# Kernel optimization log

Hardware: AMD Instinct MI355X
Metric: run time of the kernel (lower is better)

## Reference

```python
import jax, jax.numpy as jnp
import numpy as np

N = 100_000      # nodes
E = 1_600_000    # directed edges (avg degree 16)
F_IN = 128       # num_node_features
H = 8            # heads in conv1
C = 32           # hidden_channels
G = 64           # graphs in batch
NC = 10          # num_classes


def setup_inputs() -> dict:
    key = jax.random.key(0)
    ks = jax.random.split(key, 12)
    gl = lambda k, shape, fan: (jax.random.normal(k, shape, jnp.float32) / np.sqrt(fan)).astype(jnp.float32)
    return {
        "x": jax.random.normal(ks[0], (N, F_IN), jnp.float32),
        "edge_index": jax.random.randint(ks[1], (2, E), 0, N, dtype=jnp.int32),
        "batch": jnp.sort(jax.random.randint(ks[2], (N,), 0, G, dtype=jnp.int32)),
        "W1": gl(ks[3], (F_IN, H * C), F_IN),
        "att_src1": gl(ks[4], (H, C), C),
        "att_dst1": gl(ks[5], (H, C), C),
        "b1": jnp.zeros((H * C,), jnp.float32),
        "W2": gl(ks[6], (H * C, C), H * C),
        "att_src2": gl(ks[7], (1, C), C),
        "att_dst2": gl(ks[8], (1, C), C),
        "b2": jnp.zeros((C,), jnp.float32),
        "Wlin": gl(ks[9], (C, NC), C),
        "blin": jnp.zeros((NC,), jnp.float32),
    }


def gat_conv(x, src, dst, W, att_src, att_dst, bias, heads, ch, concat):
    """PyG GATConv (eval mode): gather, LeakyReLU(0.2) scores, segment softmax over dst, scatter-sum."""
    n = x.shape[0]
    h = (x @ W).reshape(n, heads, ch)                     # [N,H,C]
    a_s = jnp.sum(h * att_src, axis=-1)                   # [N,H]
    a_d = jnp.sum(h * att_dst, axis=-1)                   # [N,H]
    e = jax.nn.leaky_relu(a_s[src] + a_d[dst], 0.2)       # [E,H]
    m = jax.ops.segment_max(e, dst, num_segments=n)       # [N,H], stable softmax
    p = jnp.exp(e - m[dst])
    z = jax.ops.segment_sum(p, dst, num_segments=n)
    coef = p / (z[dst] + 1e-16)                           # [E,H]
    out = jax.ops.segment_sum(coef[:, :, None] * h[src], dst, num_segments=n)  # [N,H,C]
    out = out.reshape(n, heads * ch) if concat else out.mean(axis=1)
    return out + bias


def reference(x, edge_index, batch, W1, att_src1, att_dst1, b1,
              W2, att_src2, att_dst2, b2, Wlin, blin):
    n = x.shape[0]
    loops = jnp.arange(n, dtype=edge_index.dtype)         # GATConv add_self_loops=True
    src = jnp.concatenate([edge_index[0], loops])
    dst = jnp.concatenate([edge_index[1], loops])

    h = gat_conv(x, src, dst, W1, att_src1, att_dst1, b1, H, C, concat=True)
    h = jax.nn.elu(h)                                     # dropout is identity in eval
    h = gat_conv(h, src, dst, W2, att_src2, att_dst2, b2, 1, C, concat=False)

    # global_mean_pool over graph ids
    sums = jax.ops.segment_sum(h, batch, num_segments=G)  # [G,C]
    cnts = jax.ops.segment_sum(jnp.ones((n,), h.dtype), batch, num_segments=G)
    pooled = sums / jnp.maximum(cnts, 1.0)[:, None]

    return pooled @ Wlin + blin                           # [G,NC]
```

## Files before the change

kernel.cpp:

```cpp
#include <hip/hip_runtime.h>
#include <cstdint>

#define NN 100000
#define EE 1600000
#define GG 64
#define FIN 128
#define HC 256
#define NC 10

typedef short v8s __attribute__((ext_vector_type(8)));
typedef float v4f __attribute__((ext_vector_type(4)));
typedef unsigned short u8s __attribute__((ext_vector_type(8)));

static __device__ __forceinline__ float lrelu(float x) { return x > 0.f ? x : 0.2f * x; }
static __device__ __forceinline__ float bf2f(unsigned short b) {
  return __uint_as_float(((unsigned int)b) << 16);
}
static __device__ __forceinline__ unsigned short f2bf(float f) {
  unsigned int u = __float_as_uint(f);
  unsigned int r = (u + 0x7FFFu + ((u >> 16) & 1u)) >> 16;
  return (unsigned short)r;
}
static __device__ __forceinline__ void unpack2(unsigned int u, float& f0, float& f1) {
  f0 = __uint_as_float(u << 16);
  f1 = __uint_as_float(u & 0xFFFF0000u);
}

__global__ __launch_bounds__(256) void k_prepall(const float* __restrict__ x,
                                                 unsigned short* __restrict__ xb,
                                                 const int* __restrict__ ei,
                                                 int* __restrict__ counts,
                                                 const float* __restrict__ W1,
                                                 unsigned short* __restrict__ W1tg,
                                                 const float* __restrict__ W2,
                                                 unsigned short* __restrict__ W2thi,
                                                 unsigned short* __restrict__ W2tlo) {
  const int b = blockIdx.x;
  const int t = threadIdx.x;
  if (b < 12500) {
    const int idx = b * 256 + t;
    const int i4 = idx * 4;
    float4 v = *(const float4*)(x + i4);
    ushort4 u;
    u.x = f2bf(v.x); u.y = f2bf(v.y); u.z = f2bf(v.z); u.w = f2bf(v.w);
    *(ushort4*)(xb + i4) = u;
    if (idx < EE) atomicAdd(&counts[ei[EE + idx]], 1);
  } else if (b < 12756) {
    const int n = b - 12500;
    if (t < 128) W1tg[n * 128 + t] = f2bf(W1[t * HC + n]);
  } else {
    const int oc = b - 12756;
    float wv = W2[t * 32 + oc];
    unsigned short hi = f2bf(wv);
    W2thi[oc * 256 + t] = hi;
    W2tlo[oc * 256 + t] = f2bf(wv - bf2f(hi));
  }
}

__global__ __launch_bounds__(256) void k_gemm1(const unsigned short* __restrict__ xb,
                                               const unsigned short* __restrict__ W1tg,
                                               const float* __restrict__ att_src1,
                                               const float* __restrict__ att_dst1,
                                               unsigned short* __restrict__ h1b,
                                               float* __restrict__ as1,
                                               float* __restrict__ ad1) {
  const int t = threadIdx.x;
  const int m0 = blockIdx.x * 64;
  const int n0 = blockIdx.y * 128;
  const int hb = blockIdx.y * 4;
  const int lane = t & 63;
  const int wm = t >> 6;
  const int ml = lane & 15;
  const int quad = lane >> 4;
  int row = m0 + wm * 16 + ml; if (row >= NN) row = NN - 1;
  v4f acc[8];
#pragma unroll
  for (int tt = 0; tt < 8; ++tt) acc[tt] = (v4f){0.f, 0.f, 0.f, 0.f};
#pragma unroll
  for (int kk = 0; kk < 4; ++kk) {
    const int k0 = kk * 32 + quad * 8;
    v8s a = *(const v8s*)(xb + (size_t)row * FIN + k0);
#pragma unroll
    for (int tt = 0; tt < 8; ++tt) {
      v8s b = *(const v8s*)(W1tg + (size_t)(n0 + tt * 16 + ml) * FIN + k0);
      acc[tt] = __builtin_amdgcn_mfma_f32_16x16x32_bf16(a, b, acc[tt], 0, 0, 0);
    }
  }
#pragma unroll
  for (int tt = 0; tt < 8; ++tt) {
#pragma unroll
    for (int r = 0; r < 4; ++r) {
      int rg = m0 + wm * 16 + quad * 4 + r;
      if (rg < NN) h1b[(size_t)rg * HC + n0 + tt * 16 + ml] = f2bf(acc[tt][r]);
    }
  }
  float ps[4][4], pd[4][4];
#pragma unroll
  for (int i = 0; i < 4; ++i)
#pragma unroll
    for (int r = 0; r < 4; ++r) { ps[i][r] = 0.f; pd[i][r] = 0.f; }
#pragma unroll
  for (int i = 0; i < 4; ++i) {
#pragma unroll
    for (int half = 0; half < 2; ++half) {
      const int tt = 2 * i + half;
      const float a_s = att_src1[(hb + i) * 32 + half * 16 + ml];
      const float a_d = att_dst1[(hb + i) * 32 + half * 16 + ml];
#pragma unroll
      for (int r = 0; r < 4; ++r) {
        ps[i][r] += acc[tt][r] * a_s;
        pd[i][r] += acc[tt][r] * a_d;
      }
    }
  }
#pragma unroll
  for (int i = 0; i < 4; ++i) {
#pragma unroll
    for (int r = 0; r < 4; ++r) {
      float s = ps[i][r], d = pd[i][r];
      s += __shfl_xor(s, 1, 64); s += __shfl_xor(s, 2, 64);
      s += __shfl_xor(s, 4, 64); s += __shfl_xor(s, 8, 64);
      d += __shfl_xor(d, 1, 64); d += __shfl_xor(d, 2, 64);
      d += __shfl_xor(d, 4, 64); d += __shfl_xor(d, 8, 64);
      ps[i][r] = s; pd[i][r] = d;
    }
  }
  if (ml == 0) {
#pragma unroll
    for (int r = 0; r < 4; ++r) {
      int rg = m0 + wm * 16 + quad * 4 + r;
      if (rg < NN) {
#pragma unroll
        for (int i = 0; i < 4; ++i) {
          as1[rg * 8 + hb + i] = ps[i][r];
          ad1[rg * 8 + hb + i] = pd[i][r];
        }
      }
    }
  }
}

__global__ void k_scan1(const int* __restrict__ counts, int* __restrict__ offs,
                        int* __restrict__ bsums) {
  __shared__ int s[256];
  const int t = threadIdx.x;
  const int i = blockIdx.x * 256 + t;
  int v = (i < NN) ? counts[i] : 0;
  s[t] = v;
  __syncthreads();
  for (int off = 1; off < 256; off <<= 1) {
    int tv = (t >= off) ? s[t - off] : 0;
    __syncthreads();
    s[t] += tv;
    __syncthreads();
  }
  if (i < NN) offs[i] = s[t] - v;
  if (t == 255) bsums[blockIdx.x] = s[255];
}

__global__ void k_scan2(int* __restrict__ bsums, int nb) {
  __shared__ int s[512];
  const int t = threadIdx.x;
  int v = (t < nb) ? bsums[t] : 0;
  s[t] = v;
  __syncthreads();
  for (int off = 1; off < 512; off <<= 1) {
    int tv = (t >= off) ? s[t - off] : 0;
    __syncthreads();
    s[t] += tv;
    __syncthreads();
  }
  if (t < nb) bsums[t] = s[t] - v;
}

__global__ void k_scan3(int* __restrict__ offs, const int* __restrict__ bsums,
                        int* __restrict__ cursor) {
  const int i = blockIdx.x * 256 + threadIdx.x;
  if (i < NN) {
    int v = offs[i] + bsums[i >> 8];
    offs[i] = v;
    cursor[i] = v;
  }
  if (i == 0) offs[NN] = EE;
}

__global__ void k_scatter(const int* __restrict__ ei, int* __restrict__ cursor,
                          int* __restrict__ esrc) {
  int e = blockIdx.x * 256 + threadIdx.x;
  if (e < EE) {
    int s = ei[e];
    int d = ei[EE + e];
    int p = atomicAdd(&cursor[d], 1);
    esrc[p] = s;
  }
}

__global__ __launch_bounds__(256) void k_agg1(const unsigned short* __restrict__ h1b,
                                              const float* __restrict__ as1,
                                              const float* __restrict__ ad1,
                                              const int* __restrict__ offs,
                                              const int* __restrict__ esrc,
                                              const float* __restrict__ b1,
                                              const unsigned short* __restrict__ W2thi,
                                              const unsigned short* __restrict__ W2tlo,
                                              const float* __restrict__ att_src2,
                                              const float* __restrict__ att_dst2,
                                              unsigned short* __restrict__ h2b,
                                              float* __restrict__ as2,
                                              float* __restrict__ ad2) {
  __shared__ float wl[4][8][36];
  __shared__ __attribute__((aligned(16))) unsigned short o1hi[4][272];
  __shared__ __attribute__((aligned(16))) unsigned short o1lo[4][272];
  const int t = threadIdx.x;
  const int lane = t & 63;
  const int w = t >> 6;
  const int n0 = blockIdx.x * 4;
  const int nu = __builtin_amdgcn_readfirstlane(n0 + w);
  const int hl = lane & 31;
  const int half = lane >> 5;
  const int head = hl >> 2;
  const uint4* __restrict__ h1u4 = (const uint4*)h1b;
  const int start = offs[nu], end = offs[nu + 1];
  const float4 dnA = *(const float4*)(ad1 + (size_t)nu * 8);
  const float4 dnB = *(const float4*)(ad1 + (size_t)nu * 8 + 4);
  const float4 dn4 = (lane & 32) ? dnB : dnA;

  float z, a0, a1, a2, a3, a4, a5, a6, a7;
  {
    float w0 = __expf(lrelu(as1[nu * 8 + head] + ad1[nu * 8 + head]));
    if (half) w0 = 0.f;
    uint4 q = h1u4[(size_t)nu * 32 + hl];
    float f0, f1, f2, f3, f4, f5, f6, f7;
    unpack2(q.x, f0, f1); unpack2(q.y, f2, f3);
    unpack2(q.z, f4, f5); unpack2(q.w, f6, f7);
    z = w0;
    a0 = w0 * f0; a1 = w0 * f1; a2 = w0 * f2; a3 = w0 * f3;
    a4 = w0 * f4; a5 = w0 * f5; a6 = w0 * f6; a7 = w0 * f7;
  }
  for (int base = start; base < end; base += 32) {
    const int cnt = min(32, end - base);
    int s = 0;
    if (hl < cnt) s = esrc[base + hl];
    const int hb4 = half << 2;
    const float4 av = *(const float4*)(as1 + (size_t)s * 8 + hb4);
    float w0 = __expf(lrelu(av.x + dn4.x));
    float w1 = __expf(lrelu(av.y + dn4.y));
    float w2 = __expf(lrelu(av.z + dn4.z));
    float w3 = __expf(lrelu(av.w + dn4.w));
    const bool act = hl < cnt;
    wl[w][hb4 + 0][hl] = act ? w0 : 0.f;
    wl[w][hb4 + 1][hl] = act ? w1 : 0.f;
    wl[w][hb4 + 2][hl] = act ? w2 : 0.f;
    wl[w][hb4 + 3][hl] = act ? w3 : 0.f;
    const int cnt4 = (cnt + 3) & ~3;
    int jb = 0;
    for (; jb + 16 <= cnt4; jb += 16) {
      uint4 q[8];
#pragma unroll
      for (int u = 0; u < 8; ++u) {
        const int s0 = esrc[base + jb + 2 * u];
        const int s1 = esrc[base + jb + 2 * u + 1];
        const int sj = half ? s1 : s0;
        q[u] = h1u4[(size_t)sj * 32 + hl];
      }
#pragma unroll
      for (int u = 0; u < 8; ++u) {
        const float2 wp = *(const float2*)&wl[w][head][jb + 2 * u];
        const float we = half ? wp.y : wp.x;
        float f0, f1, f2, f3, f4, f5, f6, f7;
        unpack2(q[u].x, f0, f1); unpack2(q[u].y, f2, f3);
        unpack2(q[u].z, f4, f5); unpack2(q[u].w, f6, f7);
        z += we;
        a0 += we * f0; a1 += we * f1; a2 += we * f2; a3 += we * f3;
        a4 += we * f4; a5 += we * f5; a6 += we * f6; a7 += we * f7;
      }
    }
    for (; jb < cnt4; jb += 4) {
      uint4 q[2];
#pragma unroll
      for (int u = 0; u < 2; ++u) {
        const int s0 = esrc[base + jb + 2 * u];
        const int s1 = esrc[base + jb + 2 * u + 1];
        const int sj = half ? s1 : s0;
        q[u] = h1u4[(size_t)sj * 32 + hl];
      }
#pragma unroll
      for (int u = 0; u < 2; ++u) {
        const float2 wp = *(const float2*)&wl[w][head][jb + 2 * u];
        const float we = half ? wp.y : wp.x;
        float f0, f1, f2, f3, f4, f5, f6, f7;
        unpack2(q[u].x, f0, f1); unpack2(q[u].y, f2, f3);
        unpack2(q[u].z, f4, f5); unpack2(q[u].w, f6, f7);
        z += we;
        a0 += we * f0; a1 += we * f1; a2 += we * f2; a3 += we * f3;
        a4 += we * f4; a5 += we * f5; a6 += we * f6; a7 += we * f7;
      }
    }
  }
  a0 += __shfl_xor(a0, 32, 64); a1 += __shfl_xor(a1, 32, 64);
  a2 += __shfl_xor(a2, 32, 64); a3 += __shfl_xor(a3, 32, 64);
  a4 += __shfl_xor(a4, 32, 64); a5 += __shfl_xor(a5, 32, 64);
  a6 += __shfl_xor(a6, 32, 64); a7 += __shfl_xor(a7, 32, 64);
  z  += __shfl_xor(z, 32, 64);
  if (lane < 32) {
    const float zi = 1.0f / (z + 1e-16f);
    const float4 bb0 = *(const float4*)(b1 + 8 * hl);
    const float4 bb1 = *(const float4*)(b1 + 8 * hl + 4);
    float v0 = a0 * zi + bb0.x;
    float v1 = a1 * zi + bb0.y;
    float v2 = a2 * zi + bb0.z;
    float v3 = a3 * zi + bb0.w;
    float v4 = a4 * zi + bb1.x;
    float v5 = a5 * zi + bb1.y;
    float v6 = a6 * zi + bb1.z;
    float v7 = a7 * zi + bb1.w;
    v0 = v0 > 0.f ? v0 : (__expf(v0) - 1.0f);
    v1 = v1 > 0.f ? v1 : (__expf(v1) - 1.0f);
    v2 = v2 > 0.f ? v2 : (__expf(v2) - 1.0f);
    v3 = v3 > 0.f ? v3 : (__expf(v3) - 1.0f);
    v4 = v4 > 0.f ? v4 : (__expf(v4) - 1.0f);
    v5 = v5 > 0.f ? v5 : (__expf(v5) - 1.0f);
    v6 = v6 > 0.f ? v6 : (__expf(v6) - 1.0f);
    v7 = v7 > 0.f ? v7 : (__expf(v7) - 1.0f);
    u8s hh, ll;
    hh[0] = f2bf(v0); hh[1] = f2bf(v1); hh[2] = f2bf(v2); hh[3] = f2bf(v3);
    hh[4] = f2bf(v4); hh[5] = f2bf(v5); hh[6] = f2bf(v6); hh[7] = f2bf(v7);
    ll[0] = f2bf(v0 - bf2f(hh[0])); ll[1] = f2bf(v1 - bf2f(hh[1]));
    ll[2] = f2bf(v2 - bf2f(hh[2])); ll[3] = f2bf(v3 - bf2f(hh[3]));
    ll[4] = f2bf(v4 - bf2f(hh[4])); ll[5] = f2bf(v5 - bf2f(hh[5]));
    ll[6] = f2bf(v6 - bf2f(hh[6])); ll[7] = f2bf(v7 - bf2f(hh[7]));
    *(u8s*)&o1hi[w][8 * hl] = hh;
    *(u8s*)&o1lo[w][8 * hl] = ll;
  }
  __syncthreads();
  if (w == 0) {
    const int ml = lane & 15;
    const int quad = lane >> 4;
    const int mr = ml & 3;
    v4f acc[2];
    acc[0] = (v4f){0.f, 0.f, 0.f, 0.f};
    acc[1] = (v4f){0.f, 0.f, 0.f, 0.f};
#pragma unroll
    for (int kk = 0; kk < 8; ++kk) {
      const int k0 = kk * 32 + quad * 8;
      v8s ah = *(const v8s*)&o1hi[mr][k0];
      v8s al = *(const v8s*)&o1lo[mr][k0];
#pragma unroll
      for (int tt = 0; tt < 2; ++tt) {
        v8s bh = *(const v8s*)(W2thi + (size_t)(tt * 16 + ml) * 256 + k0);
        v8s bl = *(const v8s*)(W2tlo + (size_t)(tt * 16 + ml) * 256 + k0);
        acc[tt] = __builtin_amdgcn_mfma_f32_16x16x32_bf16(ah, bh, acc[tt], 0, 0, 0);
        acc[tt] = __builtin_amdgcn_mfma_f32_16x16x32_bf16(al, bh, acc[tt], 0, 0, 0);
        acc[tt] = __builtin_amdgcn_mfma_f32_16x16x32_bf16(ah, bl, acc[tt], 0, 0, 0);
      }
    }
    if (quad == 0) {
      const float s0 = att_src2[ml], s1 = att_src2[16 + ml];
      const float d0 = att_dst2[ml], d1 = att_dst2[16 + ml];
#pragma unroll
      for (int r = 0; r < 4; ++r) {
        const int nn = n0 + r;
        const float h0 = acc[0][r], h1v = acc[1][r];
        h2b[(size_t)nn * 32 + ml] = f2bf(h0);
        h2b[(size_t)nn * 32 + 16 + ml] = f2bf(h1v);
        float ps = h0 * s0 + h1v * s1;
        float pd = h0 * d0 + h1v * d1;
        ps += __shfl_xor(ps, 1, 64); ps += __shfl_xor(ps, 2, 64);
        ps += __shfl_xor(ps, 4, 64); ps += __shfl_xor(ps, 8, 64);
        pd += __shfl_xor(pd, 1, 64); pd += __shfl_xor(pd, 2, 64);
        pd += __shfl_xor(pd, 4, 64); pd += __shfl_xor(pd, 8, 64);
        if (ml == 0) { as2[nn] = ps; ad2[nn] = pd; }
      }
    }
  }
}

__global__ __launch_bounds__(256) void k_agg2(const unsigned short* __restrict__ h2b,
                                              const float* __restrict__ as2,
                                              const float* __restrict__ ad2,
                                              const int* __restrict__ offs,
                                              const int* __restrict__ esrc,
                                              const float* __restrict__ b2,
                                              float* __restrict__ h3) {
  __shared__ int2 swl[4][64];
  const int t = threadIdx.x;
  const int lane = t & 63;
  const int wv = t >> 6;
  const int n = __builtin_amdgcn_readfirstlane(blockIdx.x * 4 + wv);
  const int g = lane >> 3;
  const int sl = lane & 7;
  const uint2* __restrict__ h2u2 = (const uint2*)h2b;
  const int start = offs[n], end = offs[n + 1];
  const float adn = ad2[n];
  float z, c0, c1, c2, c3;
  {
    float w0 = __expf(lrelu(as2[n] + adn));
    if (g != 0) w0 = 0.f;
    uint2 q = h2u2[(size_t)n * 8 + sl];
    float f0, f1, f2, f3; unpack2(q.x, f0, f1); unpack2(q.y, f2, f3);
    z = w0; c0 = w0 * f0; c1 = w0 * f1; c2 = w0 * f2; c3 = w0 * f3;
  }
  for (int base = start; base < end; base += 64) {
    const int cnt = min(64, end - base);
    int s = 0; float wgt = 0.f;
    if (lane < cnt) {
      s = esrc[base + lane];
      wgt = __expf(lrelu(as2[s] + adn));
    }
    swl[wv][lane] = make_int2(s, __float_as_int(wgt));
    const int nit = (cnt + 15) >> 4;
#pragma unroll 2
    for (int j = 0; j < nit; ++j) {
      const int2 p0 = swl[wv][16 * j + g];
      const int2 p1 = swl[wv][16 * j + 8 + g];
      const uint2 q0 = h2u2[(size_t)p0.x * 8 + sl];
      const uint2 q1 = h2u2[(size_t)p1.x * 8 + sl];
      const float wj0 = __int_as_float(p0.y);
      const float wj1 = __int_as_float(p1.y);
      float f0, f1, f2, f3, g0, g1, g2, g3;
      unpack2(q0.x, f0, f1); unpack2(q0.y, f2, f3);
      unpack2(q1.x, g0, g1); unpack2(q1.y, g2, g3);
      z += wj0 + wj1;
      c0 += wj0 * f0; c0 += wj1 * g0;
      c1 += wj0 * f1; c1 += wj1 * g1;
      c2 += wj0 * f2; c2 += wj1 * g2;
      c3 += wj0 * f3; c3 += wj1 * g3;
    }
  }
  c0 += __shfl_xor(c0, 8, 64);  c1 += __shfl_xor(c1, 8, 64);
  c2 += __shfl_xor(c2, 8, 64);  c3 += __shfl_xor(c3, 8, 64);
  z  += __shfl_xor(z, 8, 64);
  c0 += __shfl_xor(c0, 16, 64); c1 += __shfl_xor(c1, 16, 64);
  c2 += __shfl_xor(c2, 16, 64); c3 += __shfl_xor(c3, 16, 64);
  z  += __shfl_xor(z, 16, 64);
  c0 += __shfl_xor(c0, 32, 64); c1 += __shfl_xor(c1, 32, 64);
  c2 += __shfl_xor(c2, 32, 64); c3 += __shfl_xor(c3, 32, 64);
  z  += __shfl_xor(z, 32, 64);
  if (lane < 8) {
    const float zi = 1.0f / (z + 1e-16f);
    const float4 bb = *(const float4*)(b2 + 4 * sl);
    float4 o;
    o.x = c0 * zi + bb.x;
    o.y = c1 * zi + bb.y;
    o.z = c2 * zi + bb.z;
    o.w = c3 * zi + bb.w;
    *(float4*)(h3 + (size_t)n * 32 + 4 * sl) = o;
  }
}

__global__ __launch_bounds__(256) void k_poolfin(const float* __restrict__ h3,
                                                 const int* __restrict__ batch,
                                                 const float* __restrict__ Wlin,
                                                 const float* __restrict__ blin,
                                                 float* __restrict__ out) {
  __shared__ int bounds[2];
  __shared__ float red[8][33];
  __shared__ float mean[32];
  const int g = blockIdx.x;
  const int t = threadIdx.x;
  if (t < 2) {
    int target = g + t;
    int lo = 0, hi = NN;
    while (lo < hi) { int mid = (lo + hi) >> 1; if (batch[mid] < target) lo = mid + 1; else hi = mid; }
    bounds[t] = lo;
  }
  __syncthreads();
  const int lo = bounds[0], hi = bounds[1];
  const int rr = t >> 5, c = t & 31;
  float a = 0.f;
  for (int r = lo + rr; r < hi; r += 8) a += h3[(size_t)r * 32 + c];
  red[rr][c] = a;
  __syncthreads();
  if (rr == 0) {
    float s = 0.f;
#pragma unroll
    for (int i = 0; i < 8; ++i) s += red[i][c];
    float ct = (float)(hi - lo);
    ct = ct > 1.f ? ct : 1.f;
    mean[c] = s / ct;
  }
  __syncthreads();
  if (t < NC) {
    float acc = 0.f;
#pragma unroll
    for (int cc = 0; cc < 32; ++cc) acc += mean[cc] * Wlin[cc * NC + t];
    out[g * NC + t] = acc + blin[t];
  }
}

extern "C" void kernel_launch(void* const* d_in, const int* in_sizes, int n_in,
                              void* d_out, int out_size, void* d_ws, size_t ws_size,
                              hipStream_t stream) {
  const float* x        = (const float*)d_in[0];
  const int*   ei       = (const int*)d_in[1];
  const int*   batch    = (const int*)d_in[2];
  const float* W1       = (const float*)d_in[3];
  const float* att_src1 = (const float*)d_in[4];
  const float* att_dst1 = (const float*)d_in[5];
  const float* b1       = (const float*)d_in[6];
  const float* W2       = (const float*)d_in[7];
  const float* att_src2 = (const float*)d_in[8];
  const float* att_dst2 = (const float*)d_in[9];
  const float* b2       = (const float*)d_in[10];
  const float* Wlin     = (const float*)d_in[11];
  const float* blin     = (const float*)d_in[12];
  float* out = (float*)d_out;
  char* ws = (char*)d_ws;

  unsigned short* h1b   = (unsigned short*)(ws + 0);
  unsigned short* xb    = (unsigned short*)(ws + 51200000);
  float* h3     = (float*)(ws + 51200000);
  float* as1    = (float*)(ws + 76800000);
  float* ad1    = (float*)(ws + 80000000);
  int* counts   = (int*)(ws + 83200000);
  int* offs     = (int*)(ws + 83600000);
  int* cursor   = (int*)(ws + 84000256);
  int* esrc     = (int*)(ws + 84400256);
  int* bsums    = (int*)(ws + 90800320);
  unsigned short* h2b   = (unsigned short*)(ws + 90801920);
  float* as2    = (float*)(ws + 97201920);
  float* ad2    = (float*)(ws + 97601920);
  unsigned short* W1tg  = (unsigned short*)(ws + 98001920);
  unsigned short* W2thi = (unsigned short*)(ws + 98067456);
  unsigned short* W2tlo = (unsigned short*)(ws + 98083840);

  const int nb_scan = (NN + 255) / 256;

  hipMemsetAsync(counts, 0, NN * sizeof(int), stream);
  hipMemsetAsync(ws + 90800256, 0, 64, stream);
  k_prepall<<<12788, 256, 0, stream>>>(x, xb, ei, counts, W1, W1tg, W2, W2thi, W2tlo);

  dim3 g1((NN + 63) / 64, 2);
  k_gemm1<<<g1, 256, 0, stream>>>(xb, W1tg, att_src1, att_dst1, h1b, as1, ad1);

  k_scan1<<<nb_scan, 256, 0, stream>>>(counts, offs, bsums);
  k_scan2<<<1, 512, 0, stream>>>(bsums, nb_scan);
  k_scan3<<<nb_scan, 256, 0, stream>>>(offs, bsums, cursor);
  k_scatter<<<(EE + 255) / 256, 256, 0, stream>>>(ei, cursor, esrc);

  k_agg1<<<NN / 4, 256, 0, stream>>>(h1b, as1, ad1, offs, esrc, b1, W2thi, W2tlo,
                                     att_src2, att_dst2, h2b, as2, ad2);

  k_agg2<<<NN / 4, 256, 0, stream>>>(h2b, as2, ad2, offs, esrc, b2, h3);
  k_poolfin<<<GG, 256, 0, stream>>>(h3, batch, Wlin, blin, out);
}
```

Before: 627.4 us.

## Remap agg1 lanes to one edge per wave with double-buffered gathers

```diff
diff --git a/kernel.cpp b/kernel.cpp
--- a/kernel.cpp
+++ b/kernel.cpp
@@ -10,7 +10,6 @@
 
 typedef short v8s __attribute__((ext_vector_type(8)));
 typedef float v4f __attribute__((ext_vector_type(4)));
-typedef unsigned short u8s __attribute__((ext_vector_type(8)));
 
 static __device__ __forceinline__ float lrelu(float x) { return x > 0.f ? x : 0.2f * x; }
 static __device__ __forceinline__ float bf2f(unsigned short b) {
@@ -174,7 +173,7 @@
 }
 
 __global__ void k_scan3(int* __restrict__ offs, const int* __restrict__ bsums,
-                        int* __restrict__ cursor) {
+                        int* __restrict__ cursor, int* __restrict__ esrc) {
   const int i = blockIdx.x * 256 + threadIdx.x;
   if (i < NN) {
     int v = offs[i] + bsums[i >> 8];
@@ -182,6 +181,7 @@
     cursor[i] = v;
   }
   if (i == 0) offs[NN] = EE;
+  if (blockIdx.x == 0 && threadIdx.x < 16) esrc[EE + threadIdx.x] = 0;
 }
 
 __global__ void k_scatter(const int* __restrict__ ei, int* __restrict__ cursor,
@@ -194,6 +194,28 @@
     esrc[p] = s;
   }
 }
+
+#define AGG1_GLOAD(Q, JB) do {                                        \
+    _Pragma("unroll")                                                 \
+    for (int u_ = 0; u_ < 4; ++u_) {                                  \
+      const int sj_ = esrc[base + (JB) + u_];    \
+      Q[u_] = h1u2[(size_t)sj_ * 64 + lane];                          \
+    }                                                                 \
+  } while (0)
+
+#define AGG1_CONS(Q, JB) do {                                         \
+    const float4 wq_ = *(const float4*)&wl[w][head][(JB)];            \
+    z += (wq_.x + wq_.y) + (wq_.z + wq_.w);                           \
+    float f0_, f1_, f2_, f3_;                                         \
+    unpack2(Q[0].x, f0_, f1_); unpack2(Q[0].y, f2_, f3_);             \
+    a0 += wq_.x * f0_; a1 += wq_.x * f1_; a2 += wq_.x * f2_; a3 += wq_.x * f3_; \
+    unpack2(Q[1].x, f0_, f1_); unpack2(Q[1].y, f2_, f3_);             \
+    a0 += wq_.y * f0_; a1 += wq_.y * f1_; a2 += wq_.y * f2_; a3 += wq_.y * f3_; \
+    unpack2(Q[2].x, f0_, f1_); unpack2(Q[2].y, f2_, f3_);             \
+    a0 += wq_.z * f0_; a1 += wq_.z * f1_; a2 += wq_.z * f2_; a3 += wq_.z * f3_; \
+    unpack2(Q[3].x, f0_, f1_); unpack2(Q[3].y, f2_, f3_);             \
+    a0 += wq_.w * f0_; a1 += wq_.w * f1_; a2 += wq_.w * f2_; a3 += wq_.w * f3_; \
+  } while (0)
 
 __global__ __launch_bounds__(256) void k_agg1(const unsigned short* __restrict__ h1b,
                                               const float* __restrict__ as1,
@@ -218,133 +240,83 @@
   const int nu = __builtin_amdgcn_readfirstlane(n0 + w);
   const int hl = lane & 31;
   const int half = lane >> 5;
-  const int head = hl >> 2;
-  const uint4* __restrict__ h1u4 = (const uint4*)h1b;
+  const int head = lane >> 3;
+  const uint2* __restrict__ h1u2 = (const uint2*)h1b;
   const int start = offs[nu], end = offs[nu + 1];
   const float4 dnA = *(const float4*)(ad1 + (size_t)nu * 8);
   const float4 dnB = *(const float4*)(ad1 + (size_t)nu * 8 + 4);
   const float4 dn4 = (lane & 32) ? dnB : dnA;
 
-  float z, a0, a1, a2, a3, a4, a5, a6, a7;
+  float z, a0, a1, a2, a3;
   {
     float w0 = __expf(lrelu(as1[nu * 8 + head] + ad1[nu * 8 + head]));
-    if (half) w0 = 0.f;
-    uint4 q = h1u4[(size_t)nu * 32 + hl];
-    float f0, f1, f2, f3, f4, f5, f6, f7;
-    unpack2(q.x, f0, f1); unpack2(q.y, f2, f3);
-    unpack2(q.z, f4, f5); unpack2(q.w, f6, f7);
-    z = w0;
-    a0 = w0 * f0; a1 = w0 * f1; a2 = w0 * f2; a3 = w0 * f3;
-    a4 = w0 * f4; a5 = w0 * f5; a6 = w0 * f6; a7 = w0 * f7;
+    uint2 q = h1u2[(size_t)nu * 64 + lane];
+    float f0, f1, f2, f3; unpack2(q.x, f0, f1); unpack2(q.y, f2, f3);
+    z = w0; a0 = w0 * f0; a1 = w0 * f1; a2 = w0 * f2; a3 = w0 * f3;
   }
   for (int base = start; base < end; base += 32) {
     const int cnt = min(32, end - base);
-    int s = 0;
-    if (hl < cnt) s = esrc[base + hl];
-    const int hb4 = half << 2;
-    const float4 av = *(const float4*)(as1 + (size_t)s * 8 + hb4);
-    float w0 = __expf(lrelu(av.x + dn4.x));
-    float w1 = __expf(lrelu(av.y + dn4.y));
-    float w2 = __expf(lrelu(av.z + dn4.z));
-    float w3 = __expf(lrelu(av.w + dn4.w));
-    const bool act = hl < cnt;
-    wl[w][hb4 + 0][hl] = act ? w0 : 0.f;
-    wl[w][hb4 + 1][hl] = act ? w1 : 0.f;
-    wl[w][hb4 + 2][hl] = act ? w2 : 0.f;
-    wl[w][hb4 + 3][hl] = act ? w3 : 0.f;
     const int cnt4 = (cnt + 3) & ~3;
+    uint2 qA[4], qB[4];
+    AGG1_GLOAD(qA, 0);
+    {
+      int s = 0;
+      if (hl < cnt) s = esrc[base + hl];
+      const int hb4 = half << 2;
+      const float4 av = *(const float4*)(as1 + (size_t)s * 8 + hb4);
+      float w0 = __expf(lrelu(av.x + dn4.x));
+      float w1 = __expf(lrelu(av.y + dn4.y));
+      float w2 = __expf(lrelu(av.z + dn4.z));
+      float w3 = __expf(lrelu(av.w + dn4.w));
+      const bool act = hl < cnt;
+      wl[w][hb4 + 0][hl] = act ? w0 : 0.f;
+      wl[w][hb4 + 1][hl] = act ? w1 : 0.f;
+      wl[w][hb4 + 2][hl] = act ? w2 : 0.f;
+      wl[w][hb4 + 3][hl] = act ? w3 : 0.f;
+    }
     int jb = 0;
-    for (; jb + 16 <= cnt4; jb += 16) {
-      uint4 q[8];
-#pragma unroll
-      for (int u = 0; u < 8; ++u) {
-        const int s0 = esrc[base + jb + 2 * u];
-        const int s1 = esrc[base + jb + 2 * u + 1];
-        const int sj = half ? s1 : s0;
-        q[u] = h1u4[(size_t)sj * 32 + hl];
-      }
-#pragma unroll
-      for (int u = 0; u < 8; ++u) {
-        const float2 wp = *(const float2*)&wl[w][head][jb + 2 * u];
-        const float we = half ? wp.y : wp.x;
-        float f0, f1, f2, f3, f4, f5, f6, f7;
-        unpack2(q[u].x, f0, f1); unpack2(q[u].y, f2, f3);
-        unpack2(q[u].z, f4, f5); unpack2(q[u].w, f6, f7);
-        z += we;
-        a0 += we * f0; a1 += we * f1; a2 += we * f2; a3 += we * f3;
-        a4 += we * f4; a5 += we * f5; a6 += we * f6; a7 += we * f7;
-      }
-    }
-    for (; jb < cnt4; jb += 4) {
-      uint4 q[2];
-#pragma unroll
-      for (int u = 0; u < 2; ++u) {
-        const int s0 = esrc[base + jb + 2 * u];
-        const int s1 = esrc[base + jb + 2 * u + 1];
-        const int sj = half ? s1 : s0;
-        q[u] = h1u4[(size_t)sj * 32 + hl];
-      }
-#pragma unroll
-      for (int u = 0; u < 2; ++u) {
-        const float2 wp = *(const float2*)&wl[w][head][jb + 2 * u];
-        const float we = half ? wp.y : wp.x;
-        float f0, f1, f2, f3, f4, f5, f6, f7;
-        unpack2(q[u].x, f0, f1); unpack2(q[u].y, f2, f3);
-        unpack2(q[u].z, f4, f5); unpack2(q[u].w, f6, f7);
-        z += we;
-        a0 += we * f0; a1 += we * f1; a2 += we * f2; a3 += we * f3;
-        a4 += we * f4; a5 += we * f5; a6 += we * f6; a7 += we * f7;
-      }
-    }
-  }
-  a0 += __shfl_xor(a0, 32, 64); a1 += __shfl_xor(a1, 32, 64);
-  a2 += __shfl_xor(a2, 32, 64); a3 += __shfl_xor(a3, 32, 64);
-  a4 += __shfl_xor(a4, 32, 64); a5 += __shfl_xor(a5, 32, 64);
-  a6 += __shfl_xor(a6, 32, 64); a7 += __shfl_xor(a7, 32, 64);
-  z  += __shfl_xor(z, 32, 64);
-  if (lane < 32) {
+    for (;;) {
+      if (jb + 4 < cnt4) AGG1_GLOAD(qB, jb + 4);
+      AGG1_CONS(qA, jb);
+      jb += 4;
+      if (jb >= cnt4) break;
+      if (jb + 4 < cnt4) AGG1_GLOAD(qA, jb + 4);
+      AGG1_CONS(qB, jb);
+      jb += 4;
+      if (jb >= cnt4) break;
+    }
+  }
+  {
     const float zi = 1.0f / (z + 1e-16f);
-    const float4 bb0 = *(const float4*)(b1 + 8 * hl);
-    const float4 bb1 = *(const float4*)(b1 + 8 * hl + 4);
-    float v0 = a0 * zi + bb0.x;
-    float v1 = a1 * zi + bb0.y;
-    float v2 = a2 * zi + bb0.z;
-    float v3 = a3 * zi + bb0.w;
-    float v4 = a4 * zi + bb1.x;
-    float v5 = a5 * zi + bb1.y;
-    float v6 = a6 * zi + bb1.z;
-    float v7 = a7 * zi + bb1.w;
+    const float4 bb = *(const float4*)(b1 + 4 * lane);
+    float v0 = a0 * zi + bb.x;
+    float v1 = a1 * zi + bb.y;
+    float v2 = a2 * zi + bb.z;
+    float v3 = a3 * zi + bb.w;
     v0 = v0 > 0.f ? v0 : (__expf(v0) - 1.0f);
     v1 = v1 > 0.f ? v1 : (__expf(v1) - 1.0f);
     v2 = v2 > 0.f ? v2 : (__expf(v2) - 1.0f);
     v3 = v3 > 0.f ? v3 : (__expf(v3) - 1.0f);
-    v4 = v4 > 0.f ? v4 : (__expf(v4) - 1.0f);
-    v5 = v5 > 0.f ? v5 : (__expf(v5) - 1.0f);
-    v6 = v6 > 0.f ? v6 : (__expf(v6) - 1.0f);
-    v7 = v7 > 0.f ? v7 : (__expf(v7) - 1.0f);
-    u8s hh, ll;
-    hh[0] = f2bf(v0); hh[1] = f2bf(v1); hh[2] = f2bf(v2); hh[3] = f2bf(v3);
-    hh[4] = f2bf(v4); hh[5] = f2bf(v5); hh[6] = f2bf(v6); hh[7] = f2bf(v7);
-    ll[0] = f2bf(v0 - bf2f(hh[0])); ll[1] = f2bf(v1 - bf2f(hh[1]));
-    ll[2] = f2bf(v2 - bf2f(hh[2])); ll[3] = f2bf(v3 - bf2f(hh[3]));
-    ll[4] = f2bf(v4 - bf2f(hh[4])); ll[5] = f2bf(v5 - bf2f(hh[5]));
-    ll[6] = f2bf(v6 - bf2f(hh[6])); ll[7] = f2bf(v7 - bf2f(hh[7]));
-    *(u8s*)&o1hi[w][8 * hl] = hh;
-    *(u8s*)&o1lo[w][8 * hl] = ll;
-  }
-  __syncthreads();
-  if (w == 0) {
+    ushort4 hh, ll;
+    hh.x = f2bf(v0); hh.y = f2bf(v1); hh.z = f2bf(v2); hh.w = f2bf(v3);
+    ll.x = f2bf(v0 - bf2f(hh.x));
+    ll.y = f2bf(v1 - bf2f(hh.y));
+    ll.z = f2bf(v2 - bf2f(hh.z));
+    ll.w = f2bf(v3 - bf2f(hh.w));
+    *(ushort4*)&o1hi[w][4 * lane] = hh;
+    *(ushort4*)&o1lo[w][4 * lane] = ll;
+  }
+  {
     const int ml = lane & 15;
     const int quad = lane >> 4;
-    const int mr = ml & 3;
     v4f acc[2];
     acc[0] = (v4f){0.f, 0.f, 0.f, 0.f};
     acc[1] = (v4f){0.f, 0.f, 0.f, 0.f};
 #pragma unroll
     for (int kk = 0; kk < 8; ++kk) {
       const int k0 = kk * 32 + quad * 8;
-      v8s ah = *(const v8s*)&o1hi[mr][k0];
-      v8s al = *(const v8s*)&o1lo[mr][k0];
+      v8s ah = *(const v8s*)&o1hi[w][k0];
+      v8s al = *(const v8s*)&o1lo[w][k0];
 #pragma unroll
       for (int tt = 0; tt < 2; ++tt) {
         v8s bh = *(const v8s*)(W2thi + (size_t)(tt * 16 + ml) * 256 + k0);
@@ -354,26 +326,23 @@
         acc[tt] = __builtin_amdgcn_mfma_f32_16x16x32_bf16(ah, bl, acc[tt], 0, 0, 0);
       }
     }
+    const float h0 = acc[0][0], h1v = acc[1][0];
     if (quad == 0) {
-      const float s0 = att_src2[ml], s1 = att_src2[16 + ml];
-      const float d0 = att_dst2[ml], d1 = att_dst2[16 + ml];
-#pragma unroll
-      for (int r = 0; r < 4; ++r) {
-        const int nn = n0 + r;
-        const float h0 = acc[0][r], h1v = acc[1][r];
-        h2b[(size_t)nn * 32 + ml] = f2bf(h0);
-        h2b[(size_t)nn * 32 + 16 + ml] = f2bf(h1v);
-        float ps = h0 * s0 + h1v * s1;
-        float pd = h0 * d0 + h1v * d1;
-        ps += __shfl_xor(ps, 1, 64); ps += __shfl_xor(ps, 2, 64);
-        ps += __shfl_xor(ps, 4, 64); ps += __shfl_xor(ps, 8, 64);
-        pd += __shfl_xor(pd, 1, 64); pd += __shfl_xor(pd, 2, 64);
-        pd += __shfl_xor(pd, 4, 64); pd += __shfl_xor(pd, 8, 64);
-        if (ml == 0) { as2[nn] = ps; ad2[nn] = pd; }
-      }
-    }
-  }
-}
+      h2b[(size_t)nu * 32 + ml] = f2bf(h0);
+      h2b[(size_t)nu * 32 + 16 + ml] = f2bf(h1v);
+    }
+    float ps = h0 * att_src2[ml] + h1v * att_src2[16 + ml];
+    float pd = h0 * att_dst2[ml] + h1v * att_dst2[16 + ml];
+    ps += __shfl_xor(ps, 1, 64); ps += __shfl_xor(ps, 2, 64);
+    ps += __shfl_xor(ps, 4, 64); ps += __shfl_xor(ps, 8, 64);
+    pd += __shfl_xor(pd, 1, 64); pd += __shfl_xor(pd, 2, 64);
+    pd += __shfl_xor(pd, 4, 64); pd += __shfl_xor(pd, 8, 64);
+    if (lane == 0) { as2[nu] = ps; ad2[nu] = pd; }
+  }
+}
+
+#undef AGG1_GLOAD
+#undef AGG1_CONS
 
 __global__ __launch_bounds__(256) void k_agg2(const unsigned short* __restrict__ h2b,
                                               const float* __restrict__ as2,
@@ -409,22 +378,51 @@
     }
     swl[wv][lane] = make_int2(s, __float_as_int(wgt));
     const int nit = (cnt + 15) >> 4;
-#pragma unroll 2
-    for (int j = 0; j < nit; ++j) {
-      const int2 p0 = swl[wv][16 * j + g];
-      const int2 p1 = swl[wv][16 * j + 8 + g];
-      const uint2 q0 = h2u2[(size_t)p0.x * 8 + sl];
-      const uint2 q1 = h2u2[(size_t)p1.x * 8 + sl];
-      const float wj0 = __int_as_float(p0.y);
-      const float wj1 = __int_as_float(p1.y);
-      float f0, f1, f2, f3, g0, g1, g2, g3;
-      unpack2(q0.x, f0, f1); unpack2(q0.y, f2, f3);
-      unpack2(q1.x, g0, g1); unpack2(q1.y, g2, g3);
-      z += wj0 + wj1;
-      c0 += wj0 * f0; c0 += wj1 * g0;
-      c1 += wj0 * f1; c1 += wj1 * g1;
-      c2 += wj0 * f2; c2 += wj1 * g2;
-      c3 += wj0 * f3; c3 += wj1 * g3;
+    int2 pA0 = swl[wv][g];
+    int2 pA1 = swl[wv][8 + g];
+    uint2 qA0 = h2u2[(size_t)pA0.x * 8 + sl];
+    uint2 qA1 = h2u2[(size_t)pA1.x * 8 + sl];
+    int j = 0;
+    for (;;) {
+      int2 pB0 = pA0, pB1 = pA1; uint2 qB0, qB1;
+      if (j + 1 < nit) {
+        pB0 = swl[wv][16 * (j + 1) + g];
+        pB1 = swl[wv][16 * (j + 1) + 8 + g];
+        qB0 = h2u2[(size_t)pB0.x * 8 + sl];
+        qB1 = h2u2[(size_t)pB1.x * 8 + sl];
+      }
+      {
+        const float wj0 = __int_as_float(pA0.y);
+        const float wj1 = __int_as_float(pA1.y);
+        float f0, f1, f2, f3, g0, g1, g2, g3;
+        unpack2(qA0.x, f0, f1); unpack2(qA0.y, f2, f3);
+        unpack2(qA1.x, g0, g1); unpack2(qA1.y, g2, g3);
+        z += wj0 + wj1;
+        c0 += wj0 * f0; c0 += wj1 * g0;
+        c1 += wj0 * f1; c1 += wj1 * g1;
+        c2 += wj0 * f2; c2 += wj1 * g2;
+        c3 += wj0 * f3; c3 += wj1 * g3;
+      }
+      ++j; if (j >= nit) break;
+      if (j + 1 < nit) {
+        pA0 = swl[wv][16 * (j + 1) + g];
+        pA1 = swl[wv][16 * (j + 1) + 8 + g];
+        qA0 = h2u2[(size_t)pA0.x * 8 + sl];
+        qA1 = h2u2[(size_t)pA1.x * 8 + sl];
+      }
+      {
+        const float wj0 = __int_as_float(pB0.y);
+        const float wj1 = __int_as_float(pB1.y);
+        float f0, f1, f2, f3, g0, g1, g2, g3;
+        unpack2(qB0.x, f0, f1); unpack2(qB0.y, f2, f3);
+        unpack2(qB1.x, g0, g1); unpack2(qB1.y, g2, g3);
+        z += wj0 + wj1;
+        c0 += wj0 * f0; c0 += wj1 * g0;
+        c1 += wj0 * f1; c1 += wj1 * g1;
+        c2 += wj0 * f2; c2 += wj1 * g2;
+        c3 += wj0 * f3; c3 += wj1 * g3;
+      }
+      ++j; if (j >= nit) break;
     }
   }
   c0 += __shfl_xor(c0, 8, 64);  c1 += __shfl_xor(c1, 8, 64);
@@ -527,7 +525,6 @@
   const int nb_scan = (NN + 255) / 256;
 
   hipMemsetAsync(counts, 0, NN * sizeof(int), stream);
-  hipMemsetAsync(ws + 90800256, 0, 64, stream);
   k_prepall<<<12788, 256, 0, stream>>>(x, xb, ei, counts, W1, W1tg, W2, W2thi, W2tlo);
 
   dim3 g1((NN + 63) / 64, 2);
@@ -535,7 +532,7 @@
 
   k_scan1<<<nb_scan, 256, 0, stream>>>(counts, offs, bsums);
   k_scan2<<<1, 512, 0, stream>>>(bsums, nb_scan);
-  k_scan3<<<nb_scan, 256, 0, stream>>>(offs, bsums, cursor);
+  k_scan3<<<nb_scan, 256, 0, stream>>>(offs, bsums, cursor, esrc);
   k_scatter<<<(EE + 255) / 256, 256, 0, stream>>>(ei, cursor, esrc);
 
   k_agg1<<<NN / 4, 256, 0, stream>>>(h1b, as1, ad1, offs, esrc, b1, W2thi, W2tlo,
```

Result: slower. 863.3 us (+37.6%).
